# Kernel tuning notes

Hardware: AMD Instinct MI355X
Metric: run time of the kernel (lower is better)

Reference implementation:

```python
import jax, jax.numpy as jnp
import numpy as np

N_ROI = 2000
N_CLASSES = 21            # VOC: 20 fg + background (class 0 skipped in suppression)
IMG_H, IMG_W = 600.0, 800.0
NMS_THRESH = 0.3          # use_preset('evaluate')
SCORE_THRESH = 0.05
LOC_MEAN = jnp.array([0.0, 0.0, 0.0, 0.0], jnp.float32)
LOC_STD = jnp.array([0.1, 0.1, 0.2, 0.2], jnp.float32)


def setup_inputs() -> dict:
    key = jax.random.key(0)
    k1, k2, k3, k4 = jax.random.split(key, 4)
    # rois in (y1, x1, y2, x2) with y2 > y1, x2 > x1, inside the image
    yx1 = jax.random.uniform(k1, (N_ROI, 2), jnp.float32) * jnp.array([IMG_H * 0.8, IMG_W * 0.8])
    hw = jax.random.uniform(k2, (N_ROI, 2), jnp.float32) * jnp.array([IMG_H * 0.3, IMG_W * 0.3]) + 8.0
    rois = jnp.concatenate([yx1, yx1 + hw], axis=1)
    roi_cls_locs = jax.random.normal(k3, (N_ROI, N_CLASSES * 4), jnp.float32) * 0.5
    roi_scores = jax.random.normal(k4, (N_ROI, N_CLASSES), jnp.float32) * 2.0
    scale = jnp.ones((1,), jnp.float32)
    return {"rois": rois, "roi_cls_locs": roi_cls_locs, "roi_scores": roi_scores, "scale": scale}


def loc2bbox(src_bbox, loc):
    # src_bbox, loc: [..., 4] in (y1, x1, y2, x2) / (dy, dx, dh, dw)
    h = src_bbox[..., 2] - src_bbox[..., 0]
    w = src_bbox[..., 3] - src_bbox[..., 1]
    cy = src_bbox[..., 0] + 0.5 * h
    cx = src_bbox[..., 1] + 0.5 * w
    dy, dx, dh, dw = loc[..., 0], loc[..., 1], loc[..., 2], loc[..., 3]
    ncy = dy * h + cy
    ncx = dx * w + cx
    nh = jnp.exp(dh) * h
    nw = jnp.exp(dw) * w
    return jnp.stack([ncy - 0.5 * nh, ncx - 0.5 * nw, ncy + 0.5 * nh, ncx + 0.5 * nw], axis=-1)


def pairwise_iou(b):
    # b: [N, 4] -> [N, N]
    area = (b[:, 2] - b[:, 0]) * (b[:, 3] - b[:, 1])
    ty = jnp.maximum(b[:, None, 0], b[None, :, 0])
    tx = jnp.maximum(b[:, None, 1], b[None, :, 1])
    by = jnp.minimum(b[:, None, 2], b[None, :, 2])
    bx = jnp.minimum(b[:, None, 3], b[None, :, 3])
    inter = jnp.clip(by - ty, 0.0) * jnp.clip(bx - tx, 0.0)
    return inter / (area[:, None] + area[None, :] - inter + 1e-12)


def nms_keep(boxes, scores, valid):
    # Fixed-shape NMS: returns boolean keep mask in original order.
    n = boxes.shape[0]
    order = jnp.argsort(-jnp.where(valid, scores, -jnp.inf))
    b = boxes[order]
    v = valid[order]
    iou = pairwise_iou(b)  # [N, N]
    idx = jnp.arange(n)

    def body(i, keep):
        sup = keep[i] & (iou[i] > NMS_THRESH) & (idx > i)
        return keep & ~sup

    keep_sorted = jax.lax.fori_loop(0, n, body, v)
    return jnp.zeros(n, bool).at[order].set(keep_sorted)


def reference(rois, roi_cls_locs, roi_scores, scale):
    n, c = roi_scores.shape
    mean = jnp.tile(LOC_MEAN, c)
    std = jnp.tile(LOC_STD, c)
    locs = (roi_cls_locs * std + mean).reshape(n, c, 4)
    src = jnp.broadcast_to(rois[:, None, :], (n, c, 4))
    bboxes = loc2bbox(src, locs)  # [N, C, 4]
    original_size = jnp.array([IMG_H, IMG_W], jnp.float32) / scale[0]
    bboxes = jnp.stack([
        jnp.clip(bboxes[..., 0], 0.0, original_size[0]),
        jnp.clip(bboxes[..., 1], 0.0, original_size[1]),
        jnp.clip(bboxes[..., 2], 0.0, original_size[0]),
        jnp.clip(bboxes[..., 3], 0.0, original_size[1]),
    ], axis=-1)
    prob = jax.nn.softmax(roi_scores, axis=-1)

    # drop background class 0; class-major layout [C-1, N, ...]
    boxes_c = jnp.transpose(bboxes[:, 1:, :], (1, 0, 2))  # [C-1, N, 4]
    probs_c = prob[:, 1:].T                                # [C-1, N]
    valid = probs_c > SCORE_THRESH
    keep = jax.vmap(nms_keep)(boxes_c, probs_c, valid)     # [C-1, N] bool

    out5 = jnp.where(keep[..., None],
                     jnp.concatenate([boxes_c, probs_c[..., None]], axis=-1),
                     0.0)                                  # [C-1, N, 5]
    labels = jnp.broadcast_to(jnp.arange(c - 1, dtype=jnp.int32)[:, None], keep.shape)
    return out5, keep, labels
```

## Files before the change

### kernel.cpp

```cpp
#include <hip/hip_runtime.h>
#include <math.h>

#define NROI 2000
#define NCLS 21
#define NFG  20
#define NPAD 2048

#define OFF_BOXES   0u
#define OFF_PROBS   640000u
#define OFF_SIDX    800000u
#define OFF_SBOX    963840u
#define OFF_VC      1619200u
#define OFF_KEEP    1619328u
#define OFF_MASK    1779328u

typedef unsigned long long u64;

__global__ void k_decode(const float* __restrict__ rois,
                         const float* __restrict__ locs,
                         const float* __restrict__ scores,
                         const float* __restrict__ scale,
                         float4* __restrict__ boxes,
                         float* __restrict__ probs,
                         int* __restrict__ keepw) {
#pragma clang fp contract(off)
    int n = blockIdx.x * blockDim.x + threadIdx.x;
    if (n >= NROI) return;

#pragma unroll
    for (int c = 0; c < NFG; ++c) keepw[c * NROI + n] = 0;

    float s[NCLS];
    float m = -__builtin_inff();
#pragma unroll
    for (int k = 0; k < NCLS; ++k) {
        s[k] = scores[n * NCLS + k];
        m = fmaxf(m, s[k]);
    }
    float sum = 0.0f;
#pragma unroll
    for (int k = 0; k < NCLS; ++k) {
        s[k] = expf(s[k] - m);
        sum += s[k];
    }

    float y1 = rois[n * 4 + 0], x1 = rois[n * 4 + 1];
    float y2 = rois[n * 4 + 2], x2 = rois[n * 4 + 3];
    float h = y2 - y1, w = x2 - x1;
    float cy = y1 + 0.5f * h, cx = x1 + 0.5f * w;
    float sc = scale[0];
    float oh = 600.0f / sc, ow = 800.0f / sc;

#pragma unroll
    for (int c = 1; c < NCLS; ++c) {
        float dy = locs[n * (NCLS * 4) + c * 4 + 0] * 0.1f;
        float dx = locs[n * (NCLS * 4) + c * 4 + 1] * 0.1f;
        float dh = locs[n * (NCLS * 4) + c * 4 + 2] * 0.2f;
        float dw = locs[n * (NCLS * 4) + c * 4 + 3] * 0.2f;
        float ncy = dy * h + cy;
        float ncx = dx * w + cx;
        float nh = expf(dh) * h;
        float nw = expf(dw) * w;
        float b0 = ncy - 0.5f * nh;
        float b1 = ncx - 0.5f * nw;
        float b2 = ncy + 0.5f * nh;
        float b3 = ncx + 0.5f * nw;
        b0 = fminf(fmaxf(b0, 0.0f), oh);
        b1 = fminf(fmaxf(b1, 0.0f), ow);
        b2 = fminf(fmaxf(b2, 0.0f), oh);
        b3 = fminf(fmaxf(b3, 0.0f), ow);
        int o = (c - 1) * NROI + n;
        boxes[o] = make_float4(b0, b1, b2, b3);
        probs[o] = s[c] / sum;
    }
}

#define CSW(A,B,UP) { u64 lo_ = x[A] < x[B] ? x[A] : x[B]; \
                      u64 hi_ = x[A] < x[B] ? x[B] : x[A]; \
                      x[A] = (UP) ? lo_ : hi_; x[B] = (UP) ? hi_ : lo_; }

__global__ void __launch_bounds__(256) k_sort(const float* __restrict__ probs,
                                              const float4* __restrict__ boxes,
                                              int* __restrict__ sidx,
                                              float4* __restrict__ sbox,
                                              int* __restrict__ Vc) {
    int c = blockIdx.x;
    int t = threadIdx.x;
    __shared__ u64 a[NPAD];
    __shared__ int vcount;
    if (t == 0) vcount = 0;

    u64 x[8];
    int cnt = 0;
#pragma unroll
    for (int i = 0; i < 8; ++i) {
        int e = 8 * t + i;
        unsigned int u;
        if (e < NROI) {
            float pr = probs[c * NROI + e];
            bool valid = pr > 0.05f;
            cnt += valid ? 1 : 0;
            float key = valid ? pr : -__builtin_inff();
            u = __float_as_uint(key);
        } else {
            u = __float_as_uint(-__builtin_inff());
        }
        u ^= (u >> 31) ? 0xFFFFFFFFu : 0x80000000u;
        x[i] = ((u64)(~u) << 32) | (unsigned int)e;
    }
    __syncthreads();
    if (cnt) atomicAdd(&vcount, cnt);

    CSW(0,1,true)  CSW(2,3,false) CSW(4,5,true)  CSW(6,7,false)
    CSW(0,2,true)  CSW(1,3,true)  CSW(4,6,false) CSW(5,7,false)
    CSW(0,1,true)  CSW(2,3,true)  CSW(4,5,false) CSW(6,7,false)
    {
        bool up = (t & 1) == 0;
        CSW(0,4,up) CSW(1,5,up) CSW(2,6,up) CSW(3,7,up)
        CSW(0,2,up) CSW(1,3,up) CSW(4,6,up) CSW(5,7,up)
        CSW(0,1,up) CSW(2,3,up) CSW(4,5,up) CSW(6,7,up)
    }
    for (unsigned int k = 16; k <= NPAD; k <<= 1) {
        bool up = (((unsigned int)(8 * t)) & k) == 0;
        for (unsigned int j = k >> 1; j >= 8; j >>= 1) {
            if (j >= 512) {
                __syncthreads();
#pragma unroll
                for (int i = 0; i < 8; ++i) a[8 * t + i] = x[i];
                __syncthreads();
                bool lower = ((t & (j >> 3)) == 0);
                bool takeMin = (up == lower);
#pragma unroll
                for (int i = 0; i < 8; ++i) {
                    u64 y = a[(8 * t + i) ^ j];
                    u64 mn = x[i] < y ? x[i] : y;
                    u64 mx = x[i] < y ? y : x[i];
                    x[i] = takeMin ? mn : mx;
                }
            } else {
                int lm = (int)(j >> 3);
                bool lower = ((t & lm) == 0);
                bool takeMin = (up == lower);
#pragma unroll
                for (int i = 0; i < 8; ++i) {
                    u64 y = __shfl_xor(x[i], lm, 64);
                    u64 mn = x[i] < y ? x[i] : y;
                    u64 mx = x[i] < y ? y : x[i];
                    x[i] = takeMin ? mn : mx;
                }
            }
        }
        CSW(0,4,up) CSW(1,5,up) CSW(2,6,up) CSW(3,7,up)
        CSW(0,2,up) CSW(1,3,up) CSW(4,6,up) CSW(5,7,up)
        CSW(0,1,up) CSW(2,3,up) CSW(4,5,up) CSW(6,7,up)
    }

#pragma unroll
    for (int i = 0; i < 8; ++i) {
        int e = 8 * t + i;
        u64 p = x[i];
        int orig = (int)(p & 0xFFFFFFFFu);
        sidx[c * NPAD + e] = orig;
        float4 b = (orig < NROI) ? boxes[c * NROI + orig] : make_float4(0, 0, 0, 0);
        sbox[c * NPAD + e] = b;
    }
    __syncthreads();
    if (t == 0) Vc[c] = vcount;
}

__global__ void __launch_bounds__(512) k_mask(const float4* __restrict__ sbox,
                                              const int* __restrict__ Vc,
                                              u64* __restrict__ mask) {
#pragma clang fp contract(off)
    int c = blockIdx.y;
    int V = Vc[c];
    int jb = blockIdx.x;
    int j0 = jb << 6;
    if (j0 >= V) return;
    int tid = threadIdx.x;
    int lane = tid & 63;
    int wv = tid >> 6;
    int rmax = min(V, j0 + 64);
    int smax = j0 + 64;

    __shared__ float4 lb[NPAD];
    const float4* sb = sbox + c * NPAD;
    for (int i = tid; i < smax; i += 512) lb[i] = sb[i];
    __syncthreads();

    int j = j0 + lane;
    float4 cb = lb[j];
    float areaC = (cb.z - cb.x) * (cb.w - cb.y);
    u64* mrow = mask + (size_t)(c * NPAD) * 32 + jb;

    for (int r0 = wv * 8; r0 < rmax; r0 += 64) {
#pragma unroll
        for (int k = 0; k < 8; ++k) {
            int r = r0 + k;
            bool act = r < rmax;
            float4 rb = lb[act ? r : 0];
            float areaR = (rb.z - rb.x) * (rb.w - rb.y);
            float ty = fmaxf(rb.x, cb.x);
            float tx = fmaxf(rb.y, cb.y);
            float by = fminf(rb.z, cb.z);
            float bx = fminf(rb.w, cb.w);
            float ih = fmaxf(by - ty, 0.0f);
            float iw = fmaxf(bx - tx, 0.0f);
            float inter = ih * iw;
            float denom = ((areaR + areaC) - inter) + 1e-12f;
            float iou = inter / denom;
            u64 bits = __ballot((j > r) && (iou > 0.3f));
            if (act && lane == 0) mrow[(size_t)r * 32] = bits;
        }
    }
}

__global__ void __launch_bounds__(64, 1) k_scan(const int* __restrict__ sidx,
                                                const int* __restrict__ Vc,
                                                const u64* __restrict__ mask,
                                                int* __restrict__ keepw) {
    int c = blockIdx.x;
    int V = Vc[c];
    if (V <= 0) return;
    int lane = threadIdx.x;
    int w = lane & 31;
    const u64* mbase = mask + (size_t)c * NPAD * 32;
    const int* si = sidx + c * NPAD;

    int ntiles = (V + 63) >> 6;
    u64 remv = 0;
    u64 d = mbase[(size_t)lane * 32 + 0];

    for (int t = 0; t < ntiles; ++t) {
        u64 dn = 0;
        if (t + 1 < ntiles)
            dn = mbase[(size_t)(64 * (t + 1) + lane) * 32 + (t + 1)];

        u64 pf[64];
        const u64* rp = mbase + (size_t)(64 * t) * 32 + w;
#pragma unroll
        for (int j = 0; j < 64; ++j) pf[j] = rp[(size_t)j * 32];

        u64 rv = __shfl(remv, t);
        int rem = V - 64 * t;
        u64 validm = (rem >= 64) ? ~0ULL : ((1ULL << rem) - 1ULL);
        u64 cur = (~rv) & validm;
        u64 kept = 0;
        while (cur) {
            int j = __ffsll((u64)cur) - 1;
            kept |= 1ULL << j;
            cur &= ~__shfl(d, j);
            cur &= ~(1ULL << j);
        }

        u64 acc = 0;
#pragma unroll
        for (int j = 0; j < 64; ++j) {
            u64 sel = 0ULL - ((kept >> j) & 1ULL);
            acc |= pf[j] & sel;
        }
        remv |= acc;

        int r = 64 * t + lane;
        if (r < V) keepw[c * NROI + si[r]] = (int)((kept >> lane) & 1ULL);
        d = dn;
    }
}

__global__ void k_out(const float4* __restrict__ boxes,
                      const float* __restrict__ probs,
                      const int* __restrict__ keepw,
                      float* __restrict__ out) {
    int t = blockIdx.x * blockDim.x + threadIdx.x;
    if (t >= NFG * NROI) return;
    int c = t / NROI;
    int k = keepw[t];
    float4 b = boxes[t];
    float p = probs[t];
    float* o5 = out + (size_t)t * 5;
    if (k) {
        o5[0] = b.x; o5[1] = b.y; o5[2] = b.z; o5[3] = b.w; o5[4] = p;
    } else {
        o5[0] = 0.0f; o5[1] = 0.0f; o5[2] = 0.0f; o5[3] = 0.0f; o5[4] = 0.0f;
    }
    out[NFG * NROI * 5 + t] = k ? 1.0f : 0.0f;
    out[NFG * NROI * 6 + t] = (float)c;
}

extern "C" void kernel_launch(void* const* d_in, const int* in_sizes, int n_in,
                              void* d_out, int out_size, void* d_ws, size_t ws_size,
                              hipStream_t stream) {
    const float* rois   = (const float*)d_in[0];
    const float* locs   = (const float*)d_in[1];
    const float* scores = (const float*)d_in[2];
    const float* scale  = (const float*)d_in[3];
    float* out = (float*)d_out;

    char* ws = (char*)d_ws;
    float4* boxes = (float4*)(ws + OFF_BOXES);
    float*  probs = (float*)(ws + OFF_PROBS);
    int*    sidx  = (int*)(ws + OFF_SIDX);
    float4* sbox  = (float4*)(ws + OFF_SBOX);
    int*    Vc    = (int*)(ws + OFF_VC);
    int*    keepw = (int*)(ws + OFF_KEEP);
    u64*    mask  = (u64*)(ws + OFF_MASK);

    hipLaunchKernelGGL(k_decode, dim3(32), dim3(64), 0, stream,
                       rois, locs, scores, scale, boxes, probs, keepw);
    hipLaunchKernelGGL(k_sort, dim3(NFG), dim3(256), 0, stream,
                       probs, boxes, sidx, sbox, Vc);
    hipLaunchKernelGGL(k_mask, dim3(32, NFG), dim3(512), 0, stream,
                       sbox, Vc, mask);
    hipLaunchKernelGGL(k_scan, dim3(NFG), dim3(64), 0, stream,
                       sidx, Vc, mask, keepw);
    hipLaunchKernelGGL(k_out, dim3((NFG * NROI + 255) / 256), dim3(256), 0, stream,
                       boxes, probs, keepw, out);
}
```

Baseline: 86.94 us.

## Fuse decode into sort kernel and write outputs directly from scan

```diff
diff --git a/kernel.cpp b/kernel.cpp
--- a/kernel.cpp
+++ b/kernel.cpp
@@ -5,86 +5,32 @@
 #define NCLS 21
 #define NFG  20
 #define NPAD 2048
-
-#define OFF_BOXES   0u
-#define OFF_PROBS   640000u
-#define OFF_SIDX    800000u
-#define OFF_SBOX    963840u
-#define OFF_VC      1619200u
-#define OFF_KEEP    1619328u
-#define OFF_MASK    1779328u
+#define NTOT (NFG * NROI)
+
+#define OFF_SIDX    0u
+#define OFF_SPROB   163840u
+#define OFF_SBOX    327680u
+#define OFF_VC      983040u
+#define OFF_MASK    983296u
 
 typedef unsigned long long u64;
-
-__global__ void k_decode(const float* __restrict__ rois,
-                         const float* __restrict__ locs,
-                         const float* __restrict__ scores,
-                         const float* __restrict__ scale,
-                         float4* __restrict__ boxes,
-                         float* __restrict__ probs,
-                         int* __restrict__ keepw) {
-#pragma clang fp contract(off)
-    int n = blockIdx.x * blockDim.x + threadIdx.x;
-    if (n >= NROI) return;
-
-#pragma unroll
-    for (int c = 0; c < NFG; ++c) keepw[c * NROI + n] = 0;
-
-    float s[NCLS];
-    float m = -__builtin_inff();
-#pragma unroll
-    for (int k = 0; k < NCLS; ++k) {
-        s[k] = scores[n * NCLS + k];
-        m = fmaxf(m, s[k]);
-    }
-    float sum = 0.0f;
-#pragma unroll
-    for (int k = 0; k < NCLS; ++k) {
-        s[k] = expf(s[k] - m);
-        sum += s[k];
-    }
-
-    float y1 = rois[n * 4 + 0], x1 = rois[n * 4 + 1];
-    float y2 = rois[n * 4 + 2], x2 = rois[n * 4 + 3];
-    float h = y2 - y1, w = x2 - x1;
-    float cy = y1 + 0.5f * h, cx = x1 + 0.5f * w;
-    float sc = scale[0];
-    float oh = 600.0f / sc, ow = 800.0f / sc;
-
-#pragma unroll
-    for (int c = 1; c < NCLS; ++c) {
-        float dy = locs[n * (NCLS * 4) + c * 4 + 0] * 0.1f;
-        float dx = locs[n * (NCLS * 4) + c * 4 + 1] * 0.1f;
-        float dh = locs[n * (NCLS * 4) + c * 4 + 2] * 0.2f;
-        float dw = locs[n * (NCLS * 4) + c * 4 + 3] * 0.2f;
-        float ncy = dy * h + cy;
-        float ncx = dx * w + cx;
-        float nh = expf(dh) * h;
-        float nw = expf(dw) * w;
-        float b0 = ncy - 0.5f * nh;
-        float b1 = ncx - 0.5f * nw;
-        float b2 = ncy + 0.5f * nh;
-        float b3 = ncx + 0.5f * nw;
-        b0 = fminf(fmaxf(b0, 0.0f), oh);
-        b1 = fminf(fmaxf(b1, 0.0f), ow);
-        b2 = fminf(fmaxf(b2, 0.0f), oh);
-        b3 = fminf(fmaxf(b3, 0.0f), ow);
-        int o = (c - 1) * NROI + n;
-        boxes[o] = make_float4(b0, b1, b2, b3);
-        probs[o] = s[c] / sum;
-    }
-}
 
 #define CSW(A,B,UP) { u64 lo_ = x[A] < x[B] ? x[A] : x[B]; \
                       u64 hi_ = x[A] < x[B] ? x[B] : x[A]; \
                       x[A] = (UP) ? lo_ : hi_; x[B] = (UP) ? hi_ : lo_; }
 
-__global__ void __launch_bounds__(256) k_sort(const float* __restrict__ probs,
-                                              const float4* __restrict__ boxes,
+__global__ void __launch_bounds__(256) k_sort(const float* __restrict__ rois,
+                                              const float* __restrict__ locs,
+                                              const float* __restrict__ scores,
+                                              const float* __restrict__ scale,
                                               int* __restrict__ sidx,
+                                              float* __restrict__ sprob,
                                               float4* __restrict__ sbox,
-                                              int* __restrict__ Vc) {
+                                              int* __restrict__ Vc,
+                                              float* __restrict__ out) {
+#pragma clang fp contract(off)
     int c = blockIdx.x;
+    int cc = c + 1;
     int t = threadIdx.x;
     __shared__ u64 a[NPAD];
     __shared__ int vcount;
@@ -97,7 +43,17 @@
         int e = 8 * t + i;
         unsigned int u;
         if (e < NROI) {
-            float pr = probs[c * NROI + e];
+            float s[NCLS];
+            float m = -__builtin_inff();
+#pragma unroll
+            for (int k = 0; k < NCLS; ++k) {
+                s[k] = scores[e * NCLS + k];
+                m = fmaxf(m, s[k]);
+            }
+            float sum = 0.0f;
+#pragma unroll
+            for (int k = 0; k < NCLS; ++k) sum += expf(s[k] - m);
+            float pr = expf(s[cc] - m) / sum;
             bool valid = pr > 0.05f;
             cnt += valid ? 1 : 0;
             float key = valid ? pr : -__builtin_inff();
@@ -110,6 +66,17 @@
     }
     __syncthreads();
     if (cnt) atomicAdd(&vcount, cnt);
+
+    {
+        float4 z4 = make_float4(0.f, 0.f, 0.f, 0.f);
+        float4* o5v = (float4*)out + (size_t)c * (NROI * 5 / 4);
+        for (int i = t; i < NROI * 5 / 4; i += 256) o5v[i] = z4;
+        float lc = (float)c;
+        for (int i = t; i < NROI; i += 256) {
+            out[(size_t)5 * NTOT + c * NROI + i] = 0.0f;
+            out[(size_t)6 * NTOT + c * NROI + i] = lc;
+        }
+    }
 
     CSW(0,1,true)  CSW(2,3,false) CSW(4,5,true)  CSW(6,7,false)
     CSW(0,2,true)  CSW(1,3,true)  CSW(4,6,false) CSW(5,7,false)
@@ -155,14 +122,40 @@
         CSW(0,1,up) CSW(2,3,up) CSW(4,5,up) CSW(6,7,up)
     }
 
+    float sc = scale[0];
+    float oh = 600.0f / sc, ow = 800.0f / sc;
 #pragma unroll
     for (int i = 0; i < 8; ++i) {
-        int e = 8 * t + i;
+        int slot = 8 * t + i;
         u64 p = x[i];
         int orig = (int)(p & 0xFFFFFFFFu);
-        sidx[c * NPAD + e] = orig;
-        float4 b = (orig < NROI) ? boxes[c * NROI + orig] : make_float4(0, 0, 0, 0);
-        sbox[c * NPAD + e] = b;
+        sidx[c * NPAD + slot] = orig;
+        unsigned int m_ = ~(unsigned int)(p >> 32);
+        unsigned int b_ = (m_ & 0x80000000u) ? (m_ ^ 0x80000000u) : ~m_;
+        sprob[c * NPAD + slot] = __uint_as_float(b_);
+
+        float4 bb = make_float4(0.f, 0.f, 0.f, 0.f);
+        if (orig < NROI) {
+            const float4 rr = *(const float4*)(rois + (size_t)orig * 4);
+            const float4 ll = *(const float4*)(locs + (size_t)orig * (NCLS * 4) + cc * 4);
+            float h = rr.z - rr.x, w = rr.w - rr.y;
+            float cy = rr.x + 0.5f * h, cx = rr.y + 0.5f * w;
+            float dy = ll.x * 0.1f, dx = ll.y * 0.1f;
+            float dh = ll.z * 0.2f, dw = ll.w * 0.2f;
+            float ncy = dy * h + cy;
+            float ncx = dx * w + cx;
+            float nh = expf(dh) * h;
+            float nw = expf(dw) * w;
+            float b0 = ncy - 0.5f * nh;
+            float b1 = ncx - 0.5f * nw;
+            float b2 = ncy + 0.5f * nh;
+            float b3 = ncx + 0.5f * nw;
+            bb.x = fminf(fmaxf(b0, 0.0f), oh);
+            bb.y = fminf(fmaxf(b1, 0.0f), ow);
+            bb.z = fminf(fmaxf(b2, 0.0f), oh);
+            bb.w = fminf(fmaxf(b3, 0.0f), ow);
+        }
+        sbox[c * NPAD + slot] = bb;
     }
     __syncthreads();
     if (t == 0) Vc[c] = vcount;
@@ -216,16 +209,17 @@
 }
 
 __global__ void __launch_bounds__(64, 1) k_scan(const int* __restrict__ sidx,
+                                                const float* __restrict__ sprob,
+                                                const float4* __restrict__ sbox,
                                                 const int* __restrict__ Vc,
                                                 const u64* __restrict__ mask,
-                                                int* __restrict__ keepw) {
+                                                float* __restrict__ out) {
     int c = blockIdx.x;
     int V = Vc[c];
     if (V <= 0) return;
     int lane = threadIdx.x;
     int w = lane & 31;
     const u64* mbase = mask + (size_t)c * NPAD * 32;
-    const int* si = sidx + c * NPAD;
 
     int ntiles = (V + 63) >> 6;
     u64 remv = 0;
@@ -235,6 +229,13 @@
         u64 dn = 0;
         if (t + 1 < ntiles)
             dn = mbase[(size_t)(64 * (t + 1) + lane) * 32 + (t + 1)];
+
+        int r = 64 * t + lane;
+        bool act = r < V;
+        int ri = act ? r : 0;
+        int orig = sidx[c * NPAD + ri];
+        float pr = sprob[c * NPAD + ri];
+        float4 bb = sbox[c * NPAD + ri];
 
         u64 pf[64];
         const u64* rp = mbase + (size_t)(64 * t) * 32 + w;
@@ -261,30 +262,14 @@
         }
         remv |= acc;
 
-        int r = 64 * t + lane;
-        if (r < V) keepw[c * NROI + si[r]] = (int)((kept >> lane) & 1ULL);
+        if (act && ((kept >> lane) & 1ULL)) {
+            size_t to = (size_t)c * NROI + orig;
+            float* o5 = out + to * 5;
+            o5[0] = bb.x; o5[1] = bb.y; o5[2] = bb.z; o5[3] = bb.w; o5[4] = pr;
+            out[(size_t)5 * NTOT + to] = 1.0f;
+        }
         d = dn;
     }
-}
-
-__global__ void k_out(const float4* __restrict__ boxes,
-                      const float* __restrict__ probs,
-                      const int* __restrict__ keepw,
-                      float* __restrict__ out) {
-    int t = blockIdx.x * blockDim.x + threadIdx.x;
-    if (t >= NFG * NROI) return;
-    int c = t / NROI;
-    int k = keepw[t];
-    float4 b = boxes[t];
-    float p = probs[t];
-    float* o5 = out + (size_t)t * 5;
-    if (k) {
-        o5[0] = b.x; o5[1] = b.y; o5[2] = b.z; o5[3] = b.w; o5[4] = p;
-    } else {
-        o5[0] = 0.0f; o5[1] = 0.0f; o5[2] = 0.0f; o5[3] = 0.0f; o5[4] = 0.0f;
-    }
-    out[NFG * NROI * 5 + t] = k ? 1.0f : 0.0f;
-    out[NFG * NROI * 6 + t] = (float)c;
 }
 
 extern "C" void kernel_launch(void* const* d_in, const int* in_sizes, int n_in,
@@ -297,22 +282,16 @@
     float* out = (float*)d_out;
 
     char* ws = (char*)d_ws;
-    float4* boxes = (float4*)(ws + OFF_BOXES);
-    float*  probs = (float*)(ws + OFF_PROBS);
     int*    sidx  = (int*)(ws + OFF_SIDX);
+    float*  sprob = (float*)(ws + OFF_SPROB);
     float4* sbox  = (float4*)(ws + OFF_SBOX);
     int*    Vc    = (int*)(ws + OFF_VC);
-    int*    keepw = (int*)(ws + OFF_KEEP);
     u64*    mask  = (u64*)(ws + OFF_MASK);
 
-    hipLaunchKernelGGL(k_decode, dim3(32), dim3(64), 0, stream,
-                       rois, locs, scores, scale, boxes, probs, keepw);
     hipLaunchKernelGGL(k_sort, dim3(NFG), dim3(256), 0, stream,
-                       probs, boxes, sidx, sbox, Vc);
+                       rois, locs, scores, scale, sidx, sprob, sbox, Vc, out);
     hipLaunchKernelGGL(k_mask, dim3(32, NFG), dim3(512), 0, stream,
                        sbox, Vc, mask);
     hipLaunchKernelGGL(k_scan, dim3(NFG), dim3(64), 0, stream,
-                       sidx, Vc, mask, keepw);
-    hipLaunchKernelGGL(k_out, dim3((NFG * NROI + 255) / 256), dim3(256), 0, stream,
-                       boxes, probs, keepw, out);
-}
+                       sidx, sprob, sbox, Vc, mask, out);
+}
```

Result: slower. 89.19 us (+2.6%).
